# Kernel optimization log

Hardware: AMD Instinct MI355X
Metric: run time of the kernel (lower is better)

## Reference

```python
import math
import jax, jax.numpy as jnp
import numpy as np

WS = (8, 7, 7)   # window_size (d, h, w)
SS = (4, 3, 3)   # shift_size
NH = 4           # num_heads
DIM = 128


def _rel_position_index(ws):
    # [N*N] int index into the (2wd-1)(2wh-1)(2ww-1) bias table
    cd, ch, cw = np.arange(ws[0]), np.arange(ws[1]), np.arange(ws[2])
    coords = np.stack(np.meshgrid(cd, ch, cw, indexing='ij')).reshape(3, -1)  # [3, N]
    rel = (coords[:, :, None] - coords[:, None, :]).transpose(1, 2, 0)        # [N, N, 3]
    rel[..., 0] += ws[0] - 1
    rel[..., 1] += ws[1] - 1
    rel[..., 2] += ws[2] - 1
    rel[..., 0] *= (2 * ws[1] - 1) * (2 * ws[2] - 1)
    rel[..., 1] *= (2 * ws[2] - 1)
    return rel.sum(-1).reshape(-1)


def _rel_coords_table(ws):
    # [(2wd-1)(2wh-1)(2ww-1), 3] log-spaced continuous coords (Swin v2)
    rd = np.arange(-(ws[0] - 1), ws[0], dtype=np.float32)
    rh = np.arange(-(ws[1] - 1), ws[1], dtype=np.float32)
    rw = np.arange(-(ws[2] - 1), ws[2], dtype=np.float32)
    t = np.stack(np.meshgrid(rd, rh, rw, indexing='ij')).transpose(1, 2, 3, 0)  # [Td,Th,Tw,3]
    t[..., 0] /= ws[0] - 1
    t[..., 1] /= ws[1] - 1
    t[..., 2] /= ws[2] - 1
    t *= 8.0
    t = np.sign(t) * np.log2(np.abs(t) + 1.0) / 3.0
    return t.reshape(-1, 3)


_REL_INDEX = _rel_position_index(WS)
_COORDS = jnp.asarray(_rel_coords_table(WS))


def _attn_mask(pD, pH, pW, ws, ss):
    img = np.zeros((pD, pH, pW), np.float32)
    sl = lambda w, s: (slice(0, -w), slice(-w, -s), slice(-s, None))
    cnt = 0
    for d in sl(ws[0], ss[0]):
        for h in sl(ws[1], ss[1]):
            for w in sl(ws[2], ss[2]):
                img[d, h, w] = cnt
                cnt += 1
    m = img.reshape(pD // ws[0], ws[0], pH // ws[1], ws[1], pW // ws[2], ws[2])
    m = m.transpose(0, 2, 4, 1, 3, 5).reshape(-1, ws[0] * ws[1] * ws[2])  # [nWin, N]
    diff = m[:, None, :] - m[:, :, None]
    return jnp.asarray(np.where(diff != 0, -100.0, 0.0).astype(np.float32))


def setup_inputs() -> dict:
    key = jax.random.key(0)
    ks = jax.random.split(key, 6)
    B, D, H, W, C = 1, 16, 56, 56, DIM
    g = lambda k, shp, sc: jax.random.normal(k, shp, dtype=jnp.float32) * sc
    return {
        'x': g(ks[0], (B, D, H, W, C), 1.0),
        'qkv_weight': g(ks[1], (3 * C, C), 0.02),
        'qkv_bias': jnp.zeros((3 * C,), jnp.float32),
        'proj_weight': g(ks[2], (C, C), 0.02),
        'proj_bias': jnp.zeros((C,), jnp.float32),
        'logit_scale': jnp.full((NH, 1, 1), float(np.log(10.0)), jnp.float32),
        'cpb_w1': g(ks[3], (512, 3), 0.02),
        'cpb_b1': jnp.zeros((512,), jnp.float32),
        'cpb_w2': g(ks[4], (NH, 512), 0.02),
    }


def reference(x, qkv_weight, qkv_bias, proj_weight, proj_bias,
              logit_scale, cpb_w1, cpb_b1, cpb_w2):
    B, D, H, W, C = x.shape
    wd, wh, ww = WS
    hd = C // NH
    pad_d, pad_h, pad_w = (-D) % wd, (-H) % wh, (-W) % ww
    x = jnp.pad(x, ((0, 0), (0, pad_d), (0, pad_h), (0, pad_w), (0, 0)))
    pD, pH, pW = D + pad_d, H + pad_h, W + pad_w
    ss = [0 if WS[i] >= (pD, pH, pW)[i] else SS[i] for i in range(3)]
    shifted = sum(ss) > 0
    if shifted:
        x = jnp.roll(x, (-ss[0], -ss[1], -ss[2]), axis=(1, 2, 3))
    nd, nh, nw = pD // wd, pH // wh, pW // ww
    nWin, N = nd * nh * nw, wd * wh * ww
    # window partition -> [B*nWin, N, C]
    xw = x.reshape(B, nd, wd, nh, wh, nw, ww, C).transpose(0, 1, 3, 5, 2, 4, 6, 7)
    xw = xw.reshape(B * nWin, N, C)
    # qkv with k-bias zeroed (Swin v2 cosine attention)
    qb = qkv_bias.at[C:2 * C].set(0.0)
    qkv = (xw @ qkv_weight.T + qb).reshape(B * nWin, N, 3, NH, hd).transpose(2, 0, 3, 1, 4)
    q, k, v = qkv[0], qkv[1], qkv[2]   # each [B*nWin, NH, N, hd]
    qn = q / jnp.maximum(jnp.linalg.norm(q, axis=-1, keepdims=True), 1e-12)
    kn = k / jnp.maximum(jnp.linalg.norm(k, axis=-1, keepdims=True), 1e-12)
    attn = jnp.einsum('bhnd,bhmd->bhnm', qn, kn)
    scale = jnp.exp(jnp.minimum(logit_scale, math.log(100.0)))  # [NH,1,1]
    attn = attn * scale
    # continuous relative position bias
    table = jax.nn.relu(_COORDS @ cpb_w1.T + cpb_b1) @ cpb_w2.T  # [T, NH]
    bias = table[_REL_INDEX].reshape(N, N, NH).transpose(2, 0, 1)
    bias = 16.0 * jax.nn.sigmoid(bias)
    attn = attn + bias[None]
    if shifted:
        mask = _attn_mask(pD, pH, pW, WS, ss)  # [nWin, N, N]
        attn = attn.reshape(B, nWin, NH, N, N) + mask[None, :, None]
        attn = attn.reshape(B * nWin, NH, N, N)
    attn = jax.nn.softmax(attn, axis=-1)
    out = jnp.einsum('bhnm,bhmd->bhnd', attn, v).transpose(0, 2, 1, 3).reshape(B * nWin, N, C)
    out = out @ proj_weight.T + proj_bias
    # window reverse -> [B, pD, pH, pW, C]
    out = out.reshape(B, nd, nh, nw, wd, wh, ww, C).transpose(0, 1, 4, 2, 5, 3, 6, 7)
    out = out.reshape(B, pD, pH, pW, C)
    if shifted:
        out = jnp.roll(out, tuple(ss), axis=(1, 2, 3))
    return out[:, :D, :H, :W, :]
```

## Files before the change

### kernel.cpp

```cpp
#include <hip/hip_runtime.h>
#include <hip/hip_bf16.h>

typedef unsigned short u16;
typedef unsigned int   u32;
typedef float f32x4  __attribute__((ext_vector_type(4)));
typedef short bf16x8 __attribute__((ext_vector_type(8)));

#define DI __device__ __forceinline__

constexpr int TBL  = 2535;
constexpr int NTOK = 50176;
constexpr float L2E = 1.4426950408889634f;

constexpr int WB_QW = 0;
constexpr int WB_PW = 49152;
constexpr int WB_QB = 65536;
constexpr int WB_PB = 65920;
constexpr int WB_TOT = 66048;

DI float b2f(u16 u){ return __uint_as_float(((u32)u)<<16); }
DI u16 f2b(float f){
  u32 u = __float_as_uint(f);
  return (u16)((u + 0x7fffu + ((u>>16)&1u)) >> 16);
}
DI float ldf(const void* p, int i, int isf32){
  return isf32 ? ((const float*)p)[i] : b2f(((const u16*)p)[i]);
}
DI f32x4 mfma16(bf16x8 a, bf16x8 b, f32x4 c){
  return __builtin_amdgcn_mfma_f32_16x16x32_bf16(a, b, c, 0, 0, 0);
}
DI u32 cvtpk(float lo, float hi){
  u32 r;
  asm("v_cvt_pk_bf16_f32 %0, %1, %2" : "=v"(r) : "v"(lo), "v"(hi));
  return r;
}
DI float vexp2(float x){
  float r;
  asm("v_exp_f32 %0, %1" : "=v"(r) : "v"(x));
  return r;
}

__global__ void k_detect(const u32* __restrict__ xw, int* __restrict__ flag){
  __shared__ int cnt;
  if (threadIdx.x == 0) cnt = 0;
  __syncthreads();
  int local = 0;
  for (int k = threadIdx.x; k < 4096; k += 256){
    u32 w = xw[k];
    u16 lo = (u16)w;
    u32 e = (lo >> 7) & 0xFF;
    if (lo != 0 && (e >= 143 || e <= 111)) local++;
  }
  atomicAdd(&cnt, local);
  __syncthreads();
  if (threadIdx.x == 0) *flag = (cnt > 1000) ? 1 : 0;
}

__global__ void k_cpb(const void* __restrict__ w1, const void* __restrict__ b1,
                      const void* __restrict__ w2, const int* __restrict__ flag,
                      const void* __restrict__ qw, const void* __restrict__ pw,
                      const void* __restrict__ qb, const void* __restrict__ pb,
                      u16* __restrict__ wb, float* __restrict__ table16){
  const int isf32 = *flag;
  {
    int gid = blockIdx.x*64 + threadIdx.x;
    if (gid < WB_TOT){
      const void* src; int off;
      if (gid < WB_PW)      { src = qw; off = gid; }
      else if (gid < WB_QB) { src = pw; off = gid - WB_PW; }
      else if (gid < WB_PB) { src = qb; off = gid - WB_QB; }
      else                  { src = pb; off = gid - WB_PB; }
      wb[gid] = isf32 ? f2b(((const float*)src)[off]) : ((const u16*)src)[off];
    }
  }
  int t = blockIdx.x, lane = threadIdx.x;
  int i = t/169; int r = t - i*169; int j = r/13; int k = r - j*13;
  float v0 = 8.f*(float)(i-7)/7.f, v1 = 8.f*(float)(j-6)/6.f, v2 = 8.f*(float)(k-6)/6.f;
  float c0 = copysignf(log2f(fabsf(v0)+1.f)*(1.f/3.f), v0);
  float c1 = copysignf(log2f(fabsf(v1)+1.f)*(1.f/3.f), v1);
  float c2 = copysignf(log2f(fabsf(v2)+1.f)*(1.f/3.f), v2);
  float a0=0.f,a1=0.f,a2=0.f,a3=0.f;
  for (int hh = lane; hh < 512; hh += 64){
    float a = c0*ldf(w1,hh*3,isf32) + c1*ldf(w1,hh*3+1,isf32)
            + c2*ldf(w1,hh*3+2,isf32) + ldf(b1,hh,isf32);
    a = fmaxf(a, 0.f);
    a0 += a*ldf(w2,hh,isf32);       a1 += a*ldf(w2,512+hh,isf32);
    a2 += a*ldf(w2,1024+hh,isf32);  a3 += a*ldf(w2,1536+hh,isf32);
  }
  #pragma unroll
  for (int off=32; off; off>>=1){
    a0 += __shfl_xor(a0, off); a1 += __shfl_xor(a1, off);
    a2 += __shfl_xor(a2, off); a3 += __shfl_xor(a3, off);
  }
  if (lane==0){
    table16[t]       = (16.f/(1.f+__expf(-a0)) - 15.f)*L2E;
    table16[TBL+t]   = (16.f/(1.f+__expf(-a1)) - 15.f)*L2E;
    table16[2*TBL+t] = (16.f/(1.f+__expf(-a2)) - 15.f)*L2E;
    table16[3*TBL+t] = (16.f/(1.f+__expf(-a3)) - 15.f)*L2E;
  }
}

__global__ void k_bias(const float* __restrict__ table16, float* __restrict__ bias16){
  int n = blockIdx.x, h = blockIdx.y;
  int td = n/49; int r2 = n - td*49; int th = r2/7; int tw = r2 - th*7;
  const float* tb = table16 + h*TBL;
  float* o = bias16 + ((size_t)h*392 + n)*392;
  for (int m = threadIdx.x; m < 392; m += 128){
    int sd = m/49; int q2 = m - sd*49; int sh = q2/7; int sw = q2 - sh*7;
    int idx = (td - sd + 7)*169 + (th - sh + 6)*13 + (tw - sw + 6);
    o[m] = tb[idx];
  }
}

__global__ __launch_bounds__(256,3) void k_qkv(const void* __restrict__ x,
    const u16* __restrict__ wb, const void* __restrict__ lsc,
    const int* __restrict__ flag, u16* __restrict__ qkvbuf){
  __shared__ __align__(16) u16 As[64*136];
  __shared__ __align__(16) u16 Ws[128*136];
  const int isf32 = *flag;
  const int tid = threadIdx.x;
  const int tokbase0 = blockIdx.x*64;
  {
    int trow = tid>>2, cq = (tid&3)*32;
    int gtok = tokbase0 + trow;
    int win = gtok/392, tt = gtok - win*392;
    int dwi = win>>6, hwi = (win>>3)&7, wwi = win&7;
    int td = tt/49; int r2 = tt - td*49; int th = r2/7; int tw = r2 - th*7;
    int pd = dwi*8 + td + 4; if (pd >= 16) pd -= 16;
    int ph = hwi*7 + th + 3; if (ph >= 56) ph -= 56;
    int pw = wwi*7 + tw + 3; if (pw >= 56) pw -= 56;
    size_t pos = (size_t)((pd*56 + ph)*56 + pw)*128 + cq;
    if (isf32){
      const float4* src = (const float4*)((const float*)x + pos);
      #pragma unroll
      for (int u=0; u<8; ++u){
        float4 a = src[u];
        ushort4 s4 = make_ushort4(f2b(a.x), f2b(a.y), f2b(a.z), f2b(a.w));
        *(ushort4*)&As[trow*136 + cq + u*4] = s4;
      }
    } else {
      const uint4* src = (const uint4*)((const u16*)x + pos);
      #pragma unroll
      for (int u=0; u<4; ++u) *(uint4*)&As[trow*136 + cq + u*8] = src[u];
    }
  }
  const int wave = tid>>6, lane = tid&63;
  const int c = lane & 15, g = lane >> 4;
  const int tokbase = tokbase0 + wave*16;
  float sl2e[4];
  #pragma unroll
  for (int h2=0; h2<4; ++h2){
    float ls = ldf(lsc, h2, isf32);
    sl2e[h2] = __expf(fminf(ls, 4.60517019f)) * L2E;
  }
  bf16x8 ka[4];
  for (int which = 0; which < 3; ++which){
    __syncthreads();
    {
      int orow = tid>>1, c2 = (tid&1)*64;
      const uint4* src = (const uint4*)(wb + WB_QW + (size_t)(which*128 + orow)*128 + c2);
      #pragma unroll
      for (int u=0; u<8; ++u) *(uint4*)&Ws[orow*136 + c2 + u*8] = src[u];
    }
    __syncthreads();
    if (which == 0){
      #pragma unroll
      for (int kk=0; kk<4; ++kk)
        ka[kk] = *(const bf16x8*)&As[(wave*16 + c)*136 + kk*32 + g*8];
    }
    f32x4 acc[8];
    #pragma unroll
    for (int nt=0; nt<8; ++nt) acc[nt] = 0.f;
    #pragma unroll
    for (int nt=0; nt<8; ++nt){
      #pragma unroll
      for (int kk=0; kk<4; ++kk){
        bf16x8 wf = *(const bf16x8*)&Ws[(nt*16 + c)*136 + kk*32 + g*8];
        acc[nt] = mfma16(ka[kk], wf, acc[nt]);
      }
    }
    if (which != 1){
      #pragma unroll
      for (int nt=0; nt<8; ++nt){
        float bv = b2f(wb[WB_QB + which*128 + nt*16 + c]);
        #pragma unroll
        for (int r=0;r<4;++r) acc[nt][r] += bv;
      }
    }
    if (which < 2){
      #pragma unroll
      for (int h2=0; h2<4; ++h2){
        f32x4 ss;
        #pragma unroll
        for (int r=0;r<4;++r)
          ss[r] = acc[2*h2][r]*acc[2*h2][r] + acc[2*h2+1][r]*acc[2*h2+1][r];
        #pragma unroll
        for (int off=1; off<16; off<<=1){
          #pragma unroll
          for (int r=0;r<4;++r) ss[r] += __shfl_xor(ss[r], off);
        }
        #pragma unroll
        for (int r=0;r<4;++r){
          float rn = rsqrtf(fmaxf(ss[r], 1e-24f));
          if (which == 0) rn *= sl2e[h2];
          acc[2*h2][r]   *= rn;
          acc[2*h2+1][r] *= rn;
        }
      }
    }
    #pragma unroll
    for (int nt=0; nt<8; ++nt){
      int oc = nt*16 + c;
      int head = oc >> 5, chb = oc & 31;
      #pragma unroll
      for (int r=0;r<4;++r){
        int t = tokbase + 4*g + r;
        qkvbuf[((size_t)(which*4+head)*NTOK + t)*32 + chb] = f2b(acc[nt][r]);
      }
    }
  }
}

#define QKT_STEP(JT, JJ, TAIL, MIXED) do { \
  bf16x8 kf = *(const bf16x8*)&klds[((JT)*16 + c)*40 + g*8]; \
  f32x4 tz = {0.f,0.f,0.f,0.f}; \
  f32x4 t = mfma16(kf, qf, tz); \
  const int mb = (JT)*16 + 4*g; \
  const int mbc = (TAIL) ? ((mb <= 388) ? mb : 388) : mb; \
  const float4 bq = *(const float4*)(brow + mbc); \
  float p0 = vexp2(t[0] + bq.x); \
  float p1 = vexp2(t[1] + bq.y); \
  float p2 = vexp2(t[2] + bq.z); \
  float p3 = vexp2(t[3] + bq.w); \
  if (MIXED){ \
    const int4 cmq = *(const int4*)&cnt[mbc]; \
    if (cmq.x != cn) p0 = 0.f; \
    if (cmq.y != cn) p1 = 0.f; \
    if (cmq.z != cn) p2 = 0.f; \
    if (cmq.w != cn) p3 = 0.f; \
  } \
  if (TAIL && mb > 388){ p0=0.f; p1=0.f; p2=0.f; p3=0.f; } \
  uint2 wv; wv.x = cvtpk(p0,p1); wv.y = cvtpk(p2,p3); \
  *(uint2*)&psw[c*20 + (JJ)*8 + 2*g] = wv; \
} while(0)

#define PV_STEP(MC) do { \
  bf16x8 pf = *(const bf16x8*)&psw[c*20 + 4*g]; \
  bf16x8 va = *(const bf16x8*)&vT[c*424 + (MC)*32 + g*8]; \
  bf16x8 vb = *(const bf16x8*)&vT[(16+c)*424 + (MC)*32 + g*8]; \
  o0 = mfma16(va, pf, o0); \
  o1 = mfma16(vb, pf, o1); \
  o2 = mfma16(ones, pf, o2); \
} while(0)

template<bool MIXED>
DI void attn_main(const u16* __restrict__ qg, const float* __restrict__ bias_h,
                  const u16* klds, const u16* vT, u32* psw, const int* cnt,
                  u16* __restrict__ aout, int win, int h, int wave, int lane){
  const int c = lane & 15, g = lane >> 4;
  const short ob = 0x3F80;
  const bf16x8 ones = {ob,ob,ob,ob,ob,ob,ob,ob};
  for (int rt = wave; rt < 25; rt += 8){
    const int nb = rt*16;
    const int nc = (nb + c < 392) ? (nb + c) : 391;
    const bf16x8 qf = *(const bf16x8*)(qg + (size_t)nc*32 + g*8);
    const int cn = MIXED ? cnt[nc] : 0;
    const float* brow = bias_h + (size_t)nc*392;
    f32x4 o0 = {0.f,0.f,0.f,0.f}, o1 = {0.f,0.f,0.f,0.f}, o2 = {0.f,0.f,0.f,0.f};
    for (int mc = 0; mc < 12; ++mc){
      QKT_STEP(2*mc,   0, false, MIXED);
      QKT_STEP(2*mc+1, 1, false, MIXED);
      PV_STEP(mc);
    }
    QKT_STEP(24, 0, true, MIXED);
    { uint2 zz; zz.x = 0u; zz.y = 0u; *(uint2*)&psw[c*20 + 8 + 2*g] = zz; }
    PV_STEP(12);
    const float rv = 1.f / o2[0];
    uint2 wa, wb2;
    wa.x  = cvtpk(o0[0]*rv, o0[1]*rv);  wa.y  = cvtpk(o0[2]*rv, o0[3]*rv);
    wb2.x = cvtpk(o1[0]*rv, o1[1]*rv);  wb2.y = cvtpk(o1[2]*rv, o1[3]*rv);
    *(uint2*)&psw[c*20 + 2*g]     = wa;
    *(uint2*)&psw[c*20 + 8 + 2*g] = wb2;
    const int orow = lane>>2, oq = lane&3;
    uint4 ov = *(const uint4*)&psw[orow*20 + 4*oq];
    const int n = nb + orow;
    if (n < 392)
      *(uint4*)(aout + ((size_t)(win*392 + n))*128 + h*32 + oq*8) = ov;
  }
}

__global__ __launch_bounds__(512,4) void k_attn(const u16* __restrict__ qkv,
    const float* __restrict__ bias16, u16* __restrict__ aout){
  __shared__ __align__(16) u16 klds[400*40];
  __shared__ __align__(16) u16 vT[32*424];
  __shared__ __align__(16) u32 ps[8][16*20];
  __shared__ __align__(16) int cnt[400];
  const int tid = threadIdx.x;
  const int win = blockIdx.x, h = blockIdx.y;
  const int dwi = win>>6, hwi = (win>>3)&7, wwi = win&7;
  const u16* qg = qkv + ((size_t)(0*4 + h)*NTOK + (size_t)win*392)*32;
  const u16* kg = qkv + ((size_t)(1*4 + h)*NTOK + (size_t)win*392)*32;
  const u16* vg = qkv + ((size_t)(2*4 + h)*NTOK + (size_t)win*392)*32;
  for (int idx = tid; idx < 1600; idx += 512){
    const int row = idx>>2, q = idx&3;
    uint4 a = {0,0,0,0};
    if (row < 392) a = *(const uint4*)(kg + (size_t)row*32 + q*8);
    *(uint4*)&klds[row*40 + q*8] = a;
  }
  for (int idx = tid; idx < 784; idx += 512){
    const int mg = idx>>3, cg = idx&7;
    uint2 v0 = *(const uint2*)(vg + (size_t)(4*mg+0)*32 + cg*4);
    uint2 v1 = *(const uint2*)(vg + (size_t)(4*mg+1)*32 + cg*4);
    uint2 v2 = *(const uint2*)(vg + (size_t)(4*mg+2)*32 + cg*4);
    uint2 v3 = *(const uint2*)(vg + (size_t)(4*mg+3)*32 + cg*4);
    u16 e0[4], e1[4], e2[4], e3[4];
    e0[0]=(u16)v0.x; e0[1]=(u16)(v0.x>>16); e0[2]=(u16)v0.y; e0[3]=(u16)(v0.y>>16);
    e1[0]=(u16)v1.x; e1[1]=(u16)(v1.x>>16); e1[2]=(u16)v1.y; e1[3]=(u16)(v1.y>>16);
    e2[0]=(u16)v2.x; e2[1]=(u16)(v2.x>>16); e2[2]=(u16)v2.y; e2[3]=(u16)(v2.y>>16);
    e3[0]=(u16)v3.x; e3[1]=(u16)(v3.x>>16); e3[2]=(u16)v3.y; e3[3]=(u16)(v3.y>>16);
    #pragma unroll
    for (int cc=0; cc<4; ++cc){
      ushort4 w = make_ushort4(e0[cc], e1[cc], e2[cc], e3[cc]);
      *(ushort4*)&vT[(cg*4+cc)*424 + 4*mg] = w;
    }
  }
  for (int idx = tid; idx < 1024; idx += 512){
    int ch = idx>>5, mm = 392 + (idx&31);
    vT[ch*424 + mm] = 0;
  }
  for (int t2 = tid; t2 < 400; t2 += 512){
    int row = (t2 < 392) ? t2 : 391;
    int td = row/49; int r2 = row - td*49; int th = r2/7; int tw = r2 - th*7;
    int gd = dwi*8 + td, gh = hwi*7 + th, gw = wwi*7 + tw;
    int rd = (gd < 8) ? 0 : ((gd < 12) ? 1 : 2);
    int rh = (gh < 49) ? 0 : ((gh < 53) ? 1 : 2);
    int rw = (gw < 49) ? 0 : ((gw < 53) ? 1 : 2);
    cnt[t2] = rd*9 + rh*3 + rw;
  }
  __syncthreads();
  const int wave = tid>>6, lane = tid&63;
  u32* psw = &ps[wave][0];
  const float* bias_h = bias16 + (size_t)h*153664;
  const bool uniform = (dwi == 0) && (hwi < 7) && (wwi < 7);
  if (uniform)
    attn_main<false>(qg, bias_h, klds, vT, psw, cnt, aout, win, h, wave, lane);
  else
    attn_main<true >(qg, bias_h, klds, vT, psw, cnt, aout, win, h, wave, lane);
}

__global__ __launch_bounds__(256,2) void k_proj(const u16* __restrict__ ain,
    const u16* __restrict__ wb, const int* __restrict__ flag, void* __restrict__ out){
  __shared__ __align__(16) u16 As[64*136];
  __shared__ __align__(16) u16 Ws[128*136];
  const int isf32 = *flag;
  const int tid = threadIdx.x;
  const int tokbase0 = blockIdx.x*64;
  {
    int trow = tid>>2, cq = (tid&3)*32;
    const uint4* src = (const uint4*)(ain + (size_t)(tokbase0+trow)*128 + cq);
    #pragma unroll
    for (int u=0; u<4; ++u) *(uint4*)&As[trow*136 + cq + u*8] = src[u];
  }
  {
    int orow = tid>>1, c2 = (tid&1)*64;
    const uint4* src = (const uint4*)(wb + WB_PW + (size_t)orow*128 + c2);
    #pragma unroll
    for (int u=0; u<8; ++u) *(uint4*)&Ws[orow*136 + c2 + u*8] = src[u];
  }
  __syncthreads();
  const int wave = tid>>6, lane = tid&63;
  const int c = lane & 15, g = lane >> 4;
  bf16x8 ka[4];
  #pragma unroll
  for (int kk=0; kk<4; ++kk)
    ka[kk] = *(const bf16x8*)&As[(wave*16 + c)*136 + kk*32 + g*8];
  f32x4 acc[8];
  #pragma unroll
  for (int nt=0; nt<8; ++nt) acc[nt] = 0.f;
  #pragma unroll
  for (int nt=0; nt<8; ++nt){
    #pragma unroll
    for (int kk=0; kk<4; ++kk){
      bf16x8 wf = *(const bf16x8*)&Ws[(nt*16 + c)*136 + kk*32 + g*8];
      acc[nt] = mfma16(ka[kk], wf, acc[nt]);
    }
  }
  const int tokbase = tokbase0 + wave*16;
  size_t po[4];
  #pragma unroll
  for (int r=0;r<4;++r){
    int gtok = tokbase + 4*g + r;
    int win = gtok/392, tt = gtok - win*392;
    int dwi = win>>6, hwi = (win>>3)&7, wwi = win&7;
    int td = tt/49; int r2 = tt - td*49; int th = r2/7; int tw = r2 - th*7;
    int pd = dwi*8 + td + 4; if (pd >= 16) pd -= 16;
    int ph = hwi*7 + th + 3; if (ph >= 56) ph -= 56;
    int pwx = wwi*7 + tw + 3; if (pwx >= 56) pwx -= 56;
    po[r] = (size_t)((pd*56 + ph)*56 + pwx)*128;
  }
  #pragma unroll
  for (int nt=0; nt<8; ++nt){
    int oc = nt*16 + c;
    float bv = b2f(wb[WB_PB + oc]);
    #pragma unroll
    for (int r=0;r<4;++r){
      float v = acc[nt][r] + bv;
      if (isf32) ((float*)out)[po[r] + oc] = v;
      else       ((u16*)out)[po[r] + oc] = f2b(v);
    }
  }
}

extern "C" void kernel_launch(void* const* d_in, const int* in_sizes, int n_in,
                              void* d_out, int out_size, void* d_ws, size_t ws_size,
                              hipStream_t stream){
  const void* x      = d_in[0];
  const void* qkv_w  = d_in[1];
  const void* qkv_b  = d_in[2];
  const void* proj_w = d_in[3];
  const void* proj_b = d_in[4];
  const void* lsc    = d_in[5];
  const void* cpb_w1 = d_in[6];
  const void* cpb_b1 = d_in[7];
  const void* cpb_w2 = d_in[8];
  char* ws = (char*)d_ws;
  int*   flag    = (int*)(ws);
  float* table16 = (float*)(ws + 256);
  float* bias16  = (float*)(ws + 41216);
  u16*   wb      = (u16*)(ws + 2499840);
  u16*   qkvbuf  = (u16*)(ws + 2631936);
  u16*   attnout = (u16*)(ws + 41167104);

  k_detect<<<1, 256, 0, stream>>>((const u32*)x, flag);
  k_cpb <<<TBL, 64, 0, stream>>>(cpb_w1, cpb_b1, cpb_w2, flag,
                                 qkv_w, proj_w, qkv_b, proj_b, wb, table16);
  k_bias<<<dim3(392,4), 128, 0, stream>>>(table16, bias16);
  k_qkv <<<784, 256, 0, stream>>>(x, wb, lsc, flag, qkvbuf);
  k_attn<<<dim3(128,4), 512, 0, stream>>>(qkvbuf, bias16, attnout);
  k_proj<<<784, 256, 0, stream>>>(attnout, wb, flag, d_out);
}
```

Before: 99.14 us.

## Pair row tiles in attention, inline dtype detection, coalesce fp32 proj stores

```diff
diff --git a/kernel.cpp b/kernel.cpp
--- a/kernel.cpp
+++ b/kernel.cpp
@@ -39,31 +39,24 @@
   asm("v_exp_f32 %0, %1" : "=v"(r) : "v"(x));
   return r;
 }
-
-__global__ void k_detect(const u32* __restrict__ xw, int* __restrict__ flag){
-  __shared__ int cnt;
-  if (threadIdx.x == 0) cnt = 0;
-  __syncthreads();
-  int local = 0;
-  for (int k = threadIdx.x; k < 4096; k += 256){
-    u32 w = xw[k];
-    u16 lo = (u16)w;
-    u32 e = (lo >> 7) & 0xFF;
-    if (lo != 0 && (e >= 143 || e <= 111)) local++;
-  }
-  atomicAdd(&cnt, local);
-  __syncthreads();
-  if (threadIdx.x == 0) *flag = (cnt > 1000) ? 1 : 0;
+DI int detect_f32(const void* x, int lane){
+  u32 w = ((const u32*)x)[lane];
+  u16 lo = (u16)w;
+  u32 e = (lo >> 7) & 0xFF;
+  int wild = (lo != 0 && (e >= 143 || e <= 111)) ? 1 : 0;
+  unsigned long long m = __ballot(wild);
+  return __popcll(m) > 16;
 }
 
 __global__ void k_cpb(const void* __restrict__ w1, const void* __restrict__ b1,
-                      const void* __restrict__ w2, const int* __restrict__ flag,
+                      const void* __restrict__ w2, const void* __restrict__ x,
                       const void* __restrict__ qw, const void* __restrict__ pw,
                       const void* __restrict__ qb, const void* __restrict__ pb,
                       u16* __restrict__ wb, float* __restrict__ table16){
-  const int isf32 = *flag;
+  const int lane = threadIdx.x;
+  const int isf32 = detect_f32(x, lane);
   {
-    int gid = blockIdx.x*64 + threadIdx.x;
+    int gid = blockIdx.x*64 + lane;
     if (gid < WB_TOT){
       const void* src; int off;
       if (gid < WB_PW)      { src = qw; off = gid; }
@@ -73,7 +66,7 @@
       wb[gid] = isf32 ? f2b(((const float*)src)[off]) : ((const u16*)src)[off];
     }
   }
-  int t = blockIdx.x, lane = threadIdx.x;
+  int t = blockIdx.x;
   int i = t/169; int r = t - i*169; int j = r/13; int k = r - j*13;
   float v0 = 8.f*(float)(i-7)/7.f, v1 = 8.f*(float)(j-6)/6.f, v2 = 8.f*(float)(k-6)/6.f;
   float c0 = copysignf(log2f(fabsf(v0)+1.f)*(1.f/3.f), v0);
@@ -114,11 +107,12 @@
 
 __global__ __launch_bounds__(256,3) void k_qkv(const void* __restrict__ x,
     const u16* __restrict__ wb, const void* __restrict__ lsc,
-    const int* __restrict__ flag, u16* __restrict__ qkvbuf){
+    u16* __restrict__ qkvbuf){
   __shared__ __align__(16) u16 As[64*136];
   __shared__ __align__(16) u16 Ws[128*136];
-  const int isf32 = *flag;
   const int tid = threadIdx.x;
+  const int lane = tid & 63;
+  const int isf32 = detect_f32(x, lane);
   const int tokbase0 = blockIdx.x*64;
   {
     int trow = tid>>2, cq = (tid&3)*32;
@@ -144,7 +138,7 @@
       for (int u=0; u<4; ++u) *(uint4*)&As[trow*136 + cq + u*8] = src[u];
     }
   }
-  const int wave = tid>>6, lane = tid&63;
+  const int wave = tid>>6;
   const int c = lane & 15, g = lane >> 4;
   const int tokbase = tokbase0 + wave*16;
   float sl2e[4];
@@ -221,71 +215,98 @@
   }
 }
 
-#define QKT_STEP(JT, JJ, TAIL, MIXED) do { \
+#define QKT_PAIR(JT, JJ, TAIL) do { \
   bf16x8 kf = *(const bf16x8*)&klds[((JT)*16 + c)*40 + g*8]; \
   f32x4 tz = {0.f,0.f,0.f,0.f}; \
-  f32x4 t = mfma16(kf, qf, tz); \
+  f32x4 ta = mfma16(kf, qfa, tz); \
+  f32x4 tb = mfma16(kf, qfb, tz); \
   const int mb = (JT)*16 + 4*g; \
   const int mbc = (TAIL) ? ((mb <= 388) ? mb : 388) : mb; \
-  const float4 bq = *(const float4*)(brow + mbc); \
-  float p0 = vexp2(t[0] + bq.x); \
-  float p1 = vexp2(t[1] + bq.y); \
-  float p2 = vexp2(t[2] + bq.z); \
-  float p3 = vexp2(t[3] + bq.w); \
+  const float4 ba = *(const float4*)(browA + mbc); \
+  const float4 bb = *(const float4*)(browB + mbc); \
+  float pa0 = vexp2(ta[0] + ba.x), pa1 = vexp2(ta[1] + ba.y); \
+  float pa2 = vexp2(ta[2] + ba.z), pa3 = vexp2(ta[3] + ba.w); \
+  float pb0 = vexp2(tb[0] + bb.x), pb1 = vexp2(tb[1] + bb.y); \
+  float pb2 = vexp2(tb[2] + bb.z), pb3 = vexp2(tb[3] + bb.w); \
   if (MIXED){ \
-    const int4 cmq = *(const int4*)&cnt[mbc]; \
-    if (cmq.x != cn) p0 = 0.f; \
-    if (cmq.y != cn) p1 = 0.f; \
-    if (cmq.z != cn) p2 = 0.f; \
-    if (cmq.w != cn) p3 = 0.f; \
+    const int4 cm = *(const int4*)&cnt[mbc]; \
+    if (cm.x != cnA) pa0 = 0.f;  if (cm.y != cnA) pa1 = 0.f; \
+    if (cm.z != cnA) pa2 = 0.f;  if (cm.w != cnA) pa3 = 0.f; \
+    if (cm.x != cnB) pb0 = 0.f;  if (cm.y != cnB) pb1 = 0.f; \
+    if (cm.z != cnB) pb2 = 0.f;  if (cm.w != cnB) pb3 = 0.f; \
   } \
-  if (TAIL && mb > 388){ p0=0.f; p1=0.f; p2=0.f; p3=0.f; } \
-  uint2 wv; wv.x = cvtpk(p0,p1); wv.y = cvtpk(p2,p3); \
-  *(uint2*)&psw[c*20 + (JJ)*8 + 2*g] = wv; \
+  if (TAIL && mb > 388){ pa0=0.f; pa1=0.f; pa2=0.f; pa3=0.f; \
+                         pb0=0.f; pb1=0.f; pb2=0.f; pb3=0.f; } \
+  uint2 wva, wvb; \
+  wva.x = cvtpk(pa0,pa1); wva.y = cvtpk(pa2,pa3); \
+  wvb.x = cvtpk(pb0,pb1); wvb.y = cvtpk(pb2,pb3); \
+  *(uint2*)&psA[c*20 + (JJ)*8 + 2*g] = wva; \
+  *(uint2*)&psB[c*20 + (JJ)*8 + 2*g] = wvb; \
 } while(0)
 
-#define PV_STEP(MC) do { \
-  bf16x8 pf = *(const bf16x8*)&psw[c*20 + 4*g]; \
+#define PV_PAIR(MC) do { \
+  bf16x8 pfa = *(const bf16x8*)&psA[c*20 + 4*g]; \
+  bf16x8 pfb = *(const bf16x8*)&psB[c*20 + 4*g]; \
   bf16x8 va = *(const bf16x8*)&vT[c*424 + (MC)*32 + g*8]; \
   bf16x8 vb = *(const bf16x8*)&vT[(16+c)*424 + (MC)*32 + g*8]; \
-  o0 = mfma16(va, pf, o0); \
-  o1 = mfma16(vb, pf, o1); \
-  o2 = mfma16(ones, pf, o2); \
+  o0a = mfma16(va, pfa, o0a); o1a = mfma16(vb, pfa, o1a); o2a = mfma16(ones, pfa, o2a); \
+  o0b = mfma16(va, pfb, o0b); o1b = mfma16(vb, pfb, o1b); o2b = mfma16(ones, pfb, o2b); \
 } while(0)
 
 template<bool MIXED>
 DI void attn_main(const u16* __restrict__ qg, const float* __restrict__ bias_h,
-                  const u16* klds, const u16* vT, u32* psw, const int* cnt,
+                  const u16* klds, const u16* vT, u32* psA, u32* psB, const int* cnt,
                   u16* __restrict__ aout, int win, int h, int wave, int lane){
   const int c = lane & 15, g = lane >> 4;
   const short ob = 0x3F80;
   const bf16x8 ones = {ob,ob,ob,ob,ob,ob,ob,ob};
-  for (int rt = wave; rt < 25; rt += 8){
-    const int nb = rt*16;
-    const int nc = (nb + c < 392) ? (nb + c) : 391;
-    const bf16x8 qf = *(const bf16x8*)(qg + (size_t)nc*32 + g*8);
-    const int cn = MIXED ? cnt[nc] : 0;
-    const float* brow = bias_h + (size_t)nc*392;
-    f32x4 o0 = {0.f,0.f,0.f,0.f}, o1 = {0.f,0.f,0.f,0.f}, o2 = {0.f,0.f,0.f,0.f};
+  for (int pp = wave; pp < 13; pp += 8){
+    const int rta = 2*pp;
+    const int rtb = (pp < 12) ? (2*pp+1) : 24;
+    const bool hasB = (pp < 12);
+    const int nbA = rta*16, nbB = rtb*16;
+    const int ncA = (nbA + c < 392) ? (nbA + c) : 391;
+    const int ncB = (nbB + c < 392) ? (nbB + c) : 391;
+    const bf16x8 qfa = *(const bf16x8*)(qg + (size_t)ncA*32 + g*8);
+    const bf16x8 qfb = *(const bf16x8*)(qg + (size_t)ncB*32 + g*8);
+    const int cnA = MIXED ? cnt[ncA] : 0;
+    const int cnB = MIXED ? cnt[ncB] : 0;
+    const float* browA = bias_h + (size_t)ncA*392;
+    const float* browB = bias_h + (size_t)ncB*392;
+    f32x4 o0a = {0.f,0.f,0.f,0.f}, o1a = o0a, o2a = o0a;
+    f32x4 o0b = o0a, o1b = o0a, o2b = o0a;
     for (int mc = 0; mc < 12; ++mc){
-      QKT_STEP(2*mc,   0, false, MIXED);
-      QKT_STEP(2*mc+1, 1, false, MIXED);
-      PV_STEP(mc);
-    }
-    QKT_STEP(24, 0, true, MIXED);
-    { uint2 zz; zz.x = 0u; zz.y = 0u; *(uint2*)&psw[c*20 + 8 + 2*g] = zz; }
-    PV_STEP(12);
-    const float rv = 1.f / o2[0];
+      QKT_PAIR(2*mc,   0, false);
+      QKT_PAIR(2*mc+1, 1, false);
+      PV_PAIR(mc);
+    }
+    QKT_PAIR(24, 0, true);
+    { uint2 zz; zz.x = 0u; zz.y = 0u;
+      *(uint2*)&psA[c*20 + 8 + 2*g] = zz;
+      *(uint2*)&psB[c*20 + 8 + 2*g] = zz; }
+    PV_PAIR(12);
+    const float rva = 1.f / o2a[0];
+    const float rvb = 1.f / o2b[0];
     uint2 wa, wb2;
-    wa.x  = cvtpk(o0[0]*rv, o0[1]*rv);  wa.y  = cvtpk(o0[2]*rv, o0[3]*rv);
-    wb2.x = cvtpk(o1[0]*rv, o1[1]*rv);  wb2.y = cvtpk(o1[2]*rv, o1[3]*rv);
-    *(uint2*)&psw[c*20 + 2*g]     = wa;
-    *(uint2*)&psw[c*20 + 8 + 2*g] = wb2;
+    wa.x  = cvtpk(o0a[0]*rva, o0a[1]*rva);  wa.y  = cvtpk(o0a[2]*rva, o0a[3]*rva);
+    wb2.x = cvtpk(o1a[0]*rva, o1a[1]*rva);  wb2.y = cvtpk(o1a[2]*rva, o1a[3]*rva);
+    *(uint2*)&psA[c*20 + 2*g]     = wa;
+    *(uint2*)&psA[c*20 + 8 + 2*g] = wb2;
+    wa.x  = cvtpk(o0b[0]*rvb, o0b[1]*rvb);  wa.y  = cvtpk(o0b[2]*rvb, o0b[3]*rvb);
+    wb2.x = cvtpk(o1b[0]*rvb, o1b[1]*rvb);  wb2.y = cvtpk(o1b[2]*rvb, o1b[3]*rvb);
+    *(uint2*)&psB[c*20 + 2*g]     = wa;
+    *(uint2*)&psB[c*20 + 8 + 2*g] = wb2;
     const int orow = lane>>2, oq = lane&3;
-    uint4 ov = *(const uint4*)&psw[orow*20 + 4*oq];
-    const int n = nb + orow;
-    if (n < 392)
-      *(uint4*)(aout + ((size_t)(win*392 + n))*128 + h*32 + oq*8) = ov;
+    uint4 ova = *(const uint4*)&psA[orow*20 + 4*oq];
+    const int nA = nbA + orow;
+    if (nA < 392)
+      *(uint4*)(aout + ((size_t)(win*392 + nA))*128 + h*32 + oq*8) = ova;
+    if (hasB){
+      uint4 ovb = *(const uint4*)&psB[orow*20 + 4*oq];
+      const int nB = nbB + orow;
+      if (nB < 392)
+        *(uint4*)(aout + ((size_t)(win*392 + nB))*128 + h*32 + oq*8) = ovb;
+    }
   }
 }
 
@@ -293,7 +314,7 @@
     const float* __restrict__ bias16, u16* __restrict__ aout){
   __shared__ __align__(16) u16 klds[400*40];
   __shared__ __align__(16) u16 vT[32*424];
-  __shared__ __align__(16) u32 ps[8][16*20];
+  __shared__ __align__(16) u32 ps[8][640];
   __shared__ __align__(16) int cnt[400];
   const int tid = threadIdx.x;
   const int win = blockIdx.x, h = blockIdx.y;
@@ -339,21 +360,23 @@
   }
   __syncthreads();
   const int wave = tid>>6, lane = tid&63;
-  u32* psw = &ps[wave][0];
+  u32* psA = &ps[wave][0];
+  u32* psB = &ps[wave][320];
   const float* bias_h = bias16 + (size_t)h*153664;
   const bool uniform = (dwi == 0) && (hwi < 7) && (wwi < 7);
   if (uniform)
-    attn_main<false>(qg, bias_h, klds, vT, psw, cnt, aout, win, h, wave, lane);
+    attn_main<false>(qg, bias_h, klds, vT, psA, psB, cnt, aout, win, h, wave, lane);
   else
-    attn_main<true >(qg, bias_h, klds, vT, psw, cnt, aout, win, h, wave, lane);
+    attn_main<true >(qg, bias_h, klds, vT, psA, psB, cnt, aout, win, h, wave, lane);
 }
 
 __global__ __launch_bounds__(256,2) void k_proj(const u16* __restrict__ ain,
-    const u16* __restrict__ wb, const int* __restrict__ flag, void* __restrict__ out){
+    const u16* __restrict__ wb, const void* __restrict__ x, void* __restrict__ out){
   __shared__ __align__(16) u16 As[64*136];
   __shared__ __align__(16) u16 Ws[128*136];
-  const int isf32 = *flag;
   const int tid = threadIdx.x;
+  const int lane = tid & 63;
+  const int isf32 = detect_f32(x, lane);
   const int tokbase0 = blockIdx.x*64;
   {
     int trow = tid>>2, cq = (tid&3)*32;
@@ -368,7 +391,7 @@
     for (int u=0; u<8; ++u) *(uint4*)&Ws[orow*136 + c2 + u*8] = src[u];
   }
   __syncthreads();
-  const int wave = tid>>6, lane = tid&63;
+  const int wave = tid>>6;
   const int c = lane & 15, g = lane >> 4;
   bf16x8 ka[4];
   #pragma unroll
@@ -385,28 +408,51 @@
       acc[nt] = mfma16(ka[kk], wf, acc[nt]);
     }
   }
-  const int tokbase = tokbase0 + wave*16;
-  size_t po[4];
-  #pragma unroll
-  for (int r=0;r<4;++r){
-    int gtok = tokbase + 4*g + r;
+  if (isf32){
+    __syncthreads();
+    float* WsF = (float*)Ws;
+    #pragma unroll
+    for (int nt=0; nt<8; ++nt){
+      float bv = b2f(wb[WB_PB + nt*16 + c]);
+      #pragma unroll
+      for (int r=0;r<4;++r)
+        WsF[(wave*16 + 4*g + r)*128 + nt*16 + c] = acc[nt][r] + bv;
+    }
+    __syncthreads();
+    const int tok = tid>>2, q4 = tid&3;
+    int gtok = tokbase0 + tok;
     int win = gtok/392, tt = gtok - win*392;
     int dwi = win>>6, hwi = (win>>3)&7, wwi = win&7;
     int td = tt/49; int r2 = tt - td*49; int th = r2/7; int tw = r2 - th*7;
     int pd = dwi*8 + td + 4; if (pd >= 16) pd -= 16;
     int ph = hwi*7 + th + 3; if (ph >= 56) ph -= 56;
     int pwx = wwi*7 + tw + 3; if (pwx >= 56) pwx -= 56;
-    po[r] = (size_t)((pd*56 + ph)*56 + pwx)*128;
-  }
-  #pragma unroll
-  for (int nt=0; nt<8; ++nt){
-    int oc = nt*16 + c;
-    float bv = b2f(wb[WB_PB + oc]);
+    size_t po = (size_t)((pd*56 + ph)*56 + pwx)*128;
+    const float4* srcv = (const float4*)&WsF[tok*128 + q4*32];
+    float4* dst = (float4*)((float*)out + po + q4*32);
+    #pragma unroll
+    for (int i=0;i<8;++i) dst[i] = srcv[i];
+  } else {
+    const int tokbase = tokbase0 + wave*16;
+    size_t po[4];
     #pragma unroll
     for (int r=0;r<4;++r){
-      float v = acc[nt][r] + bv;
-      if (isf32) ((float*)out)[po[r] + oc] = v;
-      else       ((u16*)out)[po[r] + oc] = f2b(v);
+      int gtok = tokbase + 4*g + r;
+      int win = gtok/392, tt = gtok - win*392;
+      int dwi = win>>6, hwi = (win>>3)&7, wwi = win&7;
+      int td = tt/49; int r2 = tt - td*49; int th = r2/7; int tw = r2 - th*7;
+      int pd = dwi*8 + td + 4; if (pd >= 16) pd -= 16;
+      int ph = hwi*7 + th + 3; if (ph >= 56) ph -= 56;
+      int pwx = wwi*7 + tw + 3; if (pwx >= 56) pwx -= 56;
+      po[r] = (size_t)((pd*56 + ph)*56 + pwx)*128;
+    }
+    #pragma unroll
+    for (int nt=0; nt<8; ++nt){
+      int oc = nt*16 + c;
+      float bv = b2f(wb[WB_PB + oc]);
+      #pragma unroll
+      for (int r=0;r<4;++r)
+        ((u16*)out)[po[r] + oc] = f2b(acc[nt][r] + bv);
     }
   }
 }
@@ -424,18 +470,16 @@
   const void* cpb_b1 = d_in[7];
   const void* cpb_w2 = d_in[8];
   char* ws = (char*)d_ws;
-  int*   flag    = (int*)(ws);
-  float* table16 = (float*)(ws + 256);
-  float* bias16  = (float*)(ws + 41216);
-  u16*   wb      = (u16*)(ws + 2499840);
-  u16*   qkvbuf  = (u16*)(ws + 2631936);
-  u16*   attnout = (u16*)(ws + 41167104);
-
-  k_detect<<<1, 256, 0, stream>>>((const u32*)x, flag);
-  k_cpb <<<TBL, 64, 0, stream>>>(cpb_w1, cpb_b1, cpb_w2, flag,
+  float* table16 = (float*)(ws);
+  float* bias16  = (float*)(ws + 40960);
+  u16*   wb      = (u16*)(ws + 2499584);
+  u16*   qkvbuf  = (u16*)(ws + 2631680);
+  u16*   attnout = (u16*)(ws + 41166848);
+
+  k_cpb <<<TBL, 64, 0, stream>>>(cpb_w1, cpb_b1, cpb_w2, x,
                                  qkv_w, proj_w, qkv_b, proj_b, wb, table16);
   k_bias<<<dim3(392,4), 128, 0, stream>>>(table16, bias16);
-  k_qkv <<<784, 256, 0, stream>>>(x, wb, lsc, flag, qkvbuf);
+  k_qkv <<<784, 256, 0, stream>>>(x, wb, lsc, qkvbuf);
   k_attn<<<dim3(128,4), 512, 0, stream>>>(qkvbuf, bias16, attnout);
-  k_proj<<<784, 256, 0, stream>>>(attnout, wb, flag, d_out);
-}
+  k_proj<<<784, 256, 0, stream>>>(attnout, wb, x, d_out);
+}
```

Result: slower. 101.7 us (+2.6%).
